# Kernel tuning notes

Hardware: AMD Instinct MI355X
Metric: run time of the kernel (lower is better)

Reference implementation:

```python
import jax, jax.numpy as jnp
import numpy as np

MASK_LOGIT_CONST = 1000000000.0
LN_EPS = 1e-12


def setup_inputs() -> dict:
    key = jax.random.key(0)
    k_in, k_w = jax.random.split(key)
    B, S, H = 8, 2048, 1024
    inputs = jax.random.normal(k_in, (B, S, H), dtype=jnp.float32)
    masks = jnp.ones((B, S, S), dtype=jnp.float32)
    w_match = jax.random.normal(k_w, (2 * H, H), dtype=jnp.float32) * (1.0 / np.sqrt(2 * H))
    b_match = jnp.zeros((H,), dtype=jnp.float32)
    ln_gamma = jnp.ones((H,), dtype=jnp.float32)
    ln_beta = jnp.zeros((H,), dtype=jnp.float32)
    return {"inputs": inputs, "masks": masks, "w_match": w_match,
            "b_match": b_match, "ln_gamma": ln_gamma, "ln_beta": ln_beta}


def reference(inputs, masks, w_match, b_match, ln_gamma, ln_beta):
    H = inputs.shape[-1]
    scale = 1.0 / jnp.sqrt(jnp.asarray(H, dtype=inputs.dtype))
    # self-attention scores [B,S,S] (dropout disabled -> query=key=inputs)
    scores = jnp.einsum('bsh,bth->bst', inputs, inputs) * scale
    # logits_mask: scores*mask + (-C)*(1-mask)
    scores = scores * masks - MASK_LOGIT_CONST * (1.0 - masks)
    probs = jax.nn.softmax(scores, axis=-1)
    context = jnp.einsum('bst,bth->bsh', probs, inputs)
    cat = jnp.concatenate([inputs, context], axis=-1)  # [B,S,2H]
    matching = jnp.einsum('bsk,kh->bsh', cat, w_match) + b_match
    # layernorm over last dim
    mu = jnp.mean(matching, axis=-1, keepdims=True)
    var = jnp.mean((matching - mu) ** 2, axis=-1, keepdims=True)
    normed = (matching - mu) * jax.lax.rsqrt(var + LN_EPS)
    return normed * ln_gamma + ln_beta
```

## Files before the change

kernel.cpp:

```cpp
#include <hip/hip_runtime.h>
#include <hip/hip_bf16.h>


typedef unsigned short ushort_t;
typedef __attribute__((ext_vector_type(8))) short short8;
typedef __attribute__((ext_vector_type(4))) float float4v;

__device__ inline float b2f(unsigned int u) {
    union { unsigned int i; float f; } v; v.i = u << 16; return v.f;
}
__device__ inline ushort_t f2b(float f) {
    __hip_bfloat16 h = __float2bfloat16(f);
    return __builtin_bit_cast(ushort_t, h);
}

__device__ inline void gload_lds16(const ushort_t* g, ushort_t* lds) {
    __builtin_amdgcn_global_load_lds(
        (const __attribute__((address_space(1))) unsigned int*)g,
        (__attribute__((address_space(3))) unsigned int*)lds, 16, 0, 0);
}

#define BM 128
#define BN 128
#define BK 64

template<int EPI>
__global__ __launch_bounds__(256, 2)
void gemm_bt(const ushort_t* __restrict__ A, const ushort_t* __restrict__ A2, int kSplit,
             const ushort_t* __restrict__ B,
             int M, int N, int K, int lda, int ldb, int ldc,
             long aBS, long bBS, long cBS,
             const float* __restrict__ mask, long mBS, float scale,
             float* __restrict__ rowsum,
             const float* __restrict__ bias,
             ushort_t* __restrict__ outb, float* __restrict__ outf)
{
    __shared__ __align__(16) ushort_t As[BM * BK];
    __shared__ __align__(16) ushort_t Bs[BN * BK];

    const int tid = threadIdx.x;
    const int z = blockIdx.z;
    A  += (size_t)z * aBS;
    A2 += (size_t)z * aBS;
    B  += (size_t)z * bBS;
    if (EPI == 1) mask += (size_t)z * mBS;
    if (EPI == 1 || EPI == 2) rowsum += (size_t)z * M;
    if (EPI != 3) outb += (size_t)z * cBS;

    const int bm = blockIdx.y * BM;
    const int bn = blockIdx.x * BN;
    const int wave = tid >> 6, lane = tid & 63;
    const int wm = (wave >> 1) * 64, wn = (wave & 1) * 64;
    const int q = lane >> 4, l15 = lane & 15;
    const int lrow = lane >> 3;
    const int cswz = (lane & 7) ^ lrow;

    float4v acc[4][4];
#pragma unroll
    for (int i = 0; i < 4; i++)
#pragma unroll
        for (int j = 0; j < 4; j++) acc[i][j] = (float4v){0.f, 0.f, 0.f, 0.f};

    for (int k0 = 0; k0 < K; k0 += BK) {
        const ushort_t* aSrc = A;
        int ka = k0;
        if (k0 >= kSplit) { aSrc = A2; ka = k0 - kSplit; }
#pragma unroll
        for (int j = 0; j < 4; j++) {
            const int p = wave * 4 + j;
            const int ro = p * 8 + lrow;
            gload_lds16(aSrc + (size_t)(bm + ro) * lda + ka + cswz * 8, &As[p * 512]);
            gload_lds16(B    + (size_t)(bn + ro) * ldb + k0 + cswz * 8, &Bs[p * 512]);
        }
        __syncthreads();
#pragma unroll
        for (int kk = 0; kk < BK; kk += 32) {
            short8 af[4], bfv[4];
#pragma unroll
            for (int mi = 0; mi < 4; mi++) {
                const int lr = wm + mi * 16 + l15;
                const int kc = (kk >> 3) + q;
                af[mi] = *(const short8*)(&As[lr * 64 + ((kc ^ (lr & 7)) << 3)]);
            }
#pragma unroll
            for (int ni = 0; ni < 4; ni++) {
                const int lr = wn + ni * 16 + l15;
                const int kc = (kk >> 3) + q;
                bfv[ni] = *(const short8*)(&Bs[lr * 64 + ((kc ^ (lr & 7)) << 3)]);
            }
#pragma unroll
            for (int mi = 0; mi < 4; mi++)
#pragma unroll
                for (int ni = 0; ni < 4; ni++)
                    acc[mi][ni] = __builtin_amdgcn_mfma_f32_16x16x32_bf16(
                        af[mi], bfv[ni], acc[mi][ni], 0, 0, 0);
        }
        __syncthreads();
    }

#pragma unroll
    for (int mi = 0; mi < 4; mi++) {
#pragma unroll
        for (int r = 0; r < 4; r++) {
            const int row = bm + wm + mi * 16 + q * 4 + r;
            const size_t ro = (size_t)row * ldc;
            float rsinv = 1.f;
            if (EPI == 2) rsinv = 1.0f / rowsum[row];
            float s = 0.f;
#pragma unroll
            for (int ni = 0; ni < 4; ni++) {
                const int col = bn + wn + ni * 16 + l15;
                float v = acc[mi][ni][r];
                if (EPI == 1) {
                    const float m = mask[(size_t)row * N + col];
                    v = __expf(v * scale * m - 1e9f * (1.0f - m));
                    s += v;
                    outb[ro + col] = f2b(v);
                } else if (EPI == 2) {
                    outb[ro + col] = f2b(v * rsinv);
                } else {
                    outf[ro + col] = v + bias[col];
                }
            }
            if (EPI == 1) {
                s += __shfl_xor(s, 8);
                s += __shfl_xor(s, 4);
                s += __shfl_xor(s, 2);
                s += __shfl_xor(s, 1);
                if (l15 == 0) atomicAdd(&rowsum[row], s);
            }
        }
    }
}

__global__ __launch_bounds__(256)
void conv_trans(const float* __restrict__ in, ushort_t* __restrict__ outT,
                ushort_t* __restrict__ outS, int R, int C)
{
    __shared__ float tile[64][65];
    const int tx = threadIdx.x & 15, ty = threadIdx.x >> 4;
    const size_t zoff = (size_t)blockIdx.z * R * C;
    const int r0 = blockIdx.y * 64, c0 = blockIdx.x * 64;
#pragma unroll
    for (int j = 0; j < 4; j++) {
        const int r = ty + j * 16;
        const float4 v = *(const float4*)(in + zoff + (size_t)(r0 + r) * C + c0 + tx * 4);
        tile[r][tx * 4 + 0] = v.x;
        tile[r][tx * 4 + 1] = v.y;
        tile[r][tx * 4 + 2] = v.z;
        tile[r][tx * 4 + 3] = v.w;
        if (outS) {
            ushort4 o;
            o.x = f2b(v.x); o.y = f2b(v.y); o.z = f2b(v.z); o.w = f2b(v.w);
            *(ushort4*)(outS + zoff + (size_t)(r0 + r) * C + c0 + tx * 4) = o;
        }
    }
    __syncthreads();
    ushort_t* tp = outT + zoff;
#pragma unroll
    for (int j = 0; j < 4; j++) {
        const int cc = ty + j * 16;
        ushort4 o;
        o.x = f2b(tile[tx * 4 + 0][cc]);
        o.y = f2b(tile[tx * 4 + 1][cc]);
        o.z = f2b(tile[tx * 4 + 2][cc]);
        o.w = f2b(tile[tx * 4 + 3][cc]);
        *(ushort4*)(tp + (size_t)(c0 + cc) * R + r0 + tx * 4) = o;
    }
}

__global__ __launch_bounds__(256)
void ln_k(const float* __restrict__ Mt, const float* __restrict__ gamma,
          const float* __restrict__ beta, float* __restrict__ out)
{
    const size_t row = blockIdx.x;
    const int tid = threadIdx.x;
    const float4 v = *(const float4*)(Mt + row * 1024 + tid * 4);
    float s  = v.x + v.y + v.z + v.w;
    float s2 = v.x * v.x + v.y * v.y + v.z * v.z + v.w * v.w;
#pragma unroll
    for (int off = 32; off > 0; off >>= 1) {
        s  += __shfl_down(s, off);
        s2 += __shfl_down(s2, off);
    }
    __shared__ float red[8];
    const int wave = tid >> 6, lane = tid & 63;
    if (lane == 0) { red[wave] = s; red[4 + wave] = s2; }
    __syncthreads();
    s  = red[0] + red[1] + red[2] + red[3];
    s2 = red[4] + red[5] + red[6] + red[7];
    const float mu  = s * (1.0f / 1024.0f);
    const float var = s2 * (1.0f / 1024.0f) - mu * mu;
    const float rinv = rsqrtf(var + 1e-12f);
    const float4 g = *(const float4*)(gamma + tid * 4);
    const float4 b = *(const float4*)(beta + tid * 4);
    float4 o;
    o.x = (v.x - mu) * rinv * g.x + b.x;
    o.y = (v.y - mu) * rinv * g.y + b.y;
    o.z = (v.z - mu) * rinv * g.z + b.z;
    o.w = (v.w - mu) * rinv * g.w + b.w;
    *(float4*)(out + row * 1024 + tid * 4) = o;
}

extern "C" void kernel_launch(void* const* d_in, const int* in_sizes, int n_in,
                              void* d_out, int out_size, void* d_ws, size_t ws_size,
                              hipStream_t stream)
{
    const float* X     = (const float*)d_in[0];
    const float* masks = (const float*)d_in[1];
    const float* Wm    = (const float*)d_in[2];
    const float* bias  = (const float*)d_in[3];
    const float* gamma = (const float*)d_in[4];
    const float* beta  = (const float*)d_in[5];
    float* out = (float*)d_out;
    char* ws = (char*)d_ws;

    const int B = 8, S = 2048, H = 1024;

    ushort_t* Xb  = (ushort_t*)(ws);
    ushort_t* XT  = (ushort_t*)(ws + 33554432);
    ushort_t* WT  = (ushort_t*)(ws + 67108864);
    ushort_t* E   = (ushort_t*)(ws + 71303168);
    float*    rs  = (float*)   (ws + 138412032);
    ushort_t* CTX = (ushort_t*)(ws + 138477568);
    float* matching = (float*)E;

    conv_trans<<<dim3(16, 32, 8), 256, 0, stream>>>(X, XT, Xb, S, H);
    conv_trans<<<dim3(16, 32, 1), 256, 0, stream>>>(Wm, WT, nullptr, 2 * H, H);
    hipMemsetAsync(rs, 0, (size_t)B * S * sizeof(float), stream);

    const float scale = 0.03125f;

    gemm_bt<1><<<dim3(16, 16, 8), 256, 0, stream>>>(
        Xb, Xb, 1 << 30, Xb,
        S, S, H, H, H, S,
        (long)S * H, (long)S * H, (long)S * S,
        masks, (long)S * S, scale, rs, nullptr, E, nullptr);

    gemm_bt<2><<<dim3(8, 16, 8), 256, 0, stream>>>(
        E, E, 1 << 30, XT,
        S, H, S, S, S, H,
        (long)S * S, (long)H * S, (long)S * H,
        nullptr, 0, 1.0f, rs, nullptr, CTX, nullptr);

    gemm_bt<3><<<dim3(8, 128, 1), 256, 0, stream>>>(
        Xb, CTX, H, WT,
        B * S, H, 2 * H, H, 2 * H, H,
        0, 0, 0,
        nullptr, 0, 1.0f, nullptr, bias, nullptr, matching);

    ln_k<<<B * S, 256, 0, stream>>>(matching, gamma, beta, out);
}
```

Baseline: 552.8 us.

## Use FP8 MFMA for score GEMM and store matching output as bf16

Quantizes X to FP8 e4m3 during the conversion pass and computes the QK^T score GEMM with a dedicated FP8 MFMA kernel (K-tile 128), keeping the fused mask/exp/rowsum epilogue. The matching GEMM now writes bf16 instead of fp32 and layernorm reads bf16, which halves that intermediate's traffic. Grid axes are swapped so blockIdx.x walks M tiles, which changes block scheduling order. FP8 scores carry much larger quantization error than bf16, and the softmax exponent amplifies it, so accuracy may suffer. The FP8 buffer reuses the CTX workspace before CTX is written.

```diff
diff --git a/kernel.cpp b/kernel.cpp
--- a/kernel.cpp
+++ b/kernel.cpp
@@ -1,5 +1,6 @@
 #include <hip/hip_runtime.h>
 #include <hip/hip_bf16.h>
+#include <hip/hip_fp8.h>
 
 
 typedef unsigned short ushort_t;
@@ -13,8 +14,11 @@
     __hip_bfloat16 h = __float2bfloat16(f);
     return __builtin_bit_cast(ushort_t, h);
 }
-
-__device__ inline void gload_lds16(const ushort_t* g, ushort_t* lds) {
+__device__ inline unsigned char f2e4(float f) {
+    return __hip_fp8_e4m3(f).__x;
+}
+
+__device__ inline void gload_lds16(const void* g, void* lds) {
     __builtin_amdgcn_global_load_lds(
         (const __attribute__((address_space(1))) unsigned int*)g,
         (__attribute__((address_space(3))) unsigned int*)lds, 16, 0, 0);
@@ -30,10 +34,9 @@
              const ushort_t* __restrict__ B,
              int M, int N, int K, int lda, int ldb, int ldc,
              long aBS, long bBS, long cBS,
-             const float* __restrict__ mask, long mBS, float scale,
-             float* __restrict__ rowsum,
+             const float* __restrict__ rowsum,
              const float* __restrict__ bias,
-             ushort_t* __restrict__ outb, float* __restrict__ outf)
+             ushort_t* __restrict__ outb)
 {
     __shared__ __align__(16) ushort_t As[BM * BK];
     __shared__ __align__(16) ushort_t Bs[BN * BK];
@@ -43,12 +46,11 @@
     A  += (size_t)z * aBS;
     A2 += (size_t)z * aBS;
     B  += (size_t)z * bBS;
-    if (EPI == 1) mask += (size_t)z * mBS;
-    if (EPI == 1 || EPI == 2) rowsum += (size_t)z * M;
-    if (EPI != 3) outb += (size_t)z * cBS;
-
-    const int bm = blockIdx.y * BM;
-    const int bn = blockIdx.x * BN;
+    if (EPI == 2) rowsum += (size_t)z * M;
+    outb += (size_t)z * cBS;
+
+    const int bm = blockIdx.x * BM;
+    const int bn = blockIdx.y * BN;
     const int wave = tid >> 6, lane = tid & 63;
     const int wm = (wave >> 1) * 64, wn = (wave & 1) * 64;
     const int q = lane >> 4, l15 = lane & 15;
@@ -76,16 +78,15 @@
 #pragma unroll
         for (int kk = 0; kk < BK; kk += 32) {
             short8 af[4], bfv[4];
+            const int kc = (kk >> 3) + q;
 #pragma unroll
             for (int mi = 0; mi < 4; mi++) {
                 const int lr = wm + mi * 16 + l15;
-                const int kc = (kk >> 3) + q;
                 af[mi] = *(const short8*)(&As[lr * 64 + ((kc ^ (lr & 7)) << 3)]);
             }
 #pragma unroll
             for (int ni = 0; ni < 4; ni++) {
                 const int lr = wn + ni * 16 + l15;
-                const int kc = (kk >> 3) + q;
                 bfv[ni] = *(const short8*)(&Bs[lr * 64 + ((kc ^ (lr & 7)) << 3)]);
             }
 #pragma unroll
@@ -106,36 +107,107 @@
             const size_t ro = (size_t)row * ldc;
             float rsinv = 1.f;
             if (EPI == 2) rsinv = 1.0f / rowsum[row];
-            float s = 0.f;
 #pragma unroll
             for (int ni = 0; ni < 4; ni++) {
                 const int col = bn + wn + ni * 16 + l15;
                 float v = acc[mi][ni][r];
-                if (EPI == 1) {
-                    const float m = mask[(size_t)row * N + col];
-                    v = __expf(v * scale * m - 1e9f * (1.0f - m));
-                    s += v;
-                    outb[ro + col] = f2b(v);
-                } else if (EPI == 2) {
-                    outb[ro + col] = f2b(v * rsinv);
-                } else {
-                    outf[ro + col] = v + bias[col];
-                }
+                if (EPI == 2) outb[ro + col] = f2b(v * rsinv);
+                else          outb[ro + col] = f2b(v + bias[col]);
             }
-            if (EPI == 1) {
-                s += __shfl_xor(s, 8);
-                s += __shfl_xor(s, 4);
-                s += __shfl_xor(s, 2);
-                s += __shfl_xor(s, 1);
-                if (l15 == 0) atomicAdd(&rowsum[row], s);
+        }
+    }
+}
+
+__global__ __launch_bounds__(256, 2)
+void gemm1_fp8(const unsigned char* __restrict__ X8,
+               const float* __restrict__ mask,
+               float* __restrict__ rowsum,
+               ushort_t* __restrict__ E)
+{
+    __shared__ __align__(16) unsigned char As[128 * 128];
+    __shared__ __align__(16) unsigned char Bs[128 * 128];
+
+    const int tid = threadIdx.x;
+    const int z = blockIdx.z;
+    const unsigned char* Xz = X8 + (size_t)z * 2048 * 1024;
+    const float* mz = mask + (size_t)z * 2048 * 2048;
+    float* rsz = rowsum + (size_t)z * 2048;
+    ushort_t* Ez = E + (size_t)z * 2048 * 2048;
+
+    const int bm = blockIdx.x * 128;
+    const int bn = blockIdx.y * 128;
+    const int wave = tid >> 6, lane = tid & 63;
+    const int wm = (wave >> 1) * 64, wn = (wave & 1) * 64;
+    const int q = lane >> 4, l15 = lane & 15;
+    const int rx = l15 & 7;
+    const int lrow = lane >> 3;
+    const int cswz = (lane & 7) ^ lrow;
+
+    float4v acc[4][4];
+#pragma unroll
+    for (int i = 0; i < 4; i++)
+#pragma unroll
+        for (int j = 0; j < 4; j++) acc[i][j] = (float4v){0.f, 0.f, 0.f, 0.f};
+
+    for (int k0 = 0; k0 < 1024; k0 += 128) {
+#pragma unroll
+        for (int j = 0; j < 4; j++) {
+            const int p = wave * 4 + j;
+            const int ro = p * 8 + lrow;
+            gload_lds16(Xz + (size_t)(bm + ro) * 1024 + k0 + cswz * 16, &As[p * 1024]);
+            gload_lds16(Xz + (size_t)(bn + ro) * 1024 + k0 + cswz * 16, &Bs[p * 1024]);
+        }
+        __syncthreads();
+#pragma unroll
+        for (int kk = 0; kk < 128; kk += 32) {
+            const int g = (kk >> 3) + q;
+            const int co = (((g >> 1) ^ rx) << 4) + ((g & 1) << 3);
+            long af[4], bfv[4];
+#pragma unroll
+            for (int mi = 0; mi < 4; mi++)
+                af[mi] = *(const long*)(&As[(wm + mi * 16 + l15) * 128 + co]);
+#pragma unroll
+            for (int ni = 0; ni < 4; ni++)
+                bfv[ni] = *(const long*)(&Bs[(wn + ni * 16 + l15) * 128 + co]);
+#pragma unroll
+            for (int mi = 0; mi < 4; mi++)
+#pragma unroll
+                for (int ni = 0; ni < 4; ni++)
+                    acc[mi][ni] = __builtin_amdgcn_mfma_f32_16x16x32_fp8_fp8(
+                        af[mi], bfv[ni], acc[mi][ni], 0, 0, 0);
+        }
+        __syncthreads();
+    }
+
+    const float scale = 0.03125f;
+#pragma unroll
+    for (int mi = 0; mi < 4; mi++) {
+#pragma unroll
+        for (int r = 0; r < 4; r++) {
+            const int row = bm + wm + mi * 16 + q * 4 + r;
+            const size_t ro = (size_t)row * 2048;
+            float s = 0.f;
+#pragma unroll
+            for (int ni = 0; ni < 4; ni++) {
+                const int col = bn + wn + ni * 16 + l15;
+                const float m = mz[ro + col];
+                float v = __expf(acc[mi][ni][r] * scale * m - 1e9f * (1.0f - m));
+                s += v;
+                Ez[ro + col] = f2b(v);
             }
+            s += __shfl_xor(s, 8);
+            s += __shfl_xor(s, 4);
+            s += __shfl_xor(s, 2);
+            s += __shfl_xor(s, 1);
+            if (l15 == 0) atomicAdd(&rsz[row], s);
         }
     }
 }
 
 __global__ __launch_bounds__(256)
 void conv_trans(const float* __restrict__ in, ushort_t* __restrict__ outT,
-                ushort_t* __restrict__ outS, int R, int C)
+                ushort_t* __restrict__ outS, unsigned char* __restrict__ outQ,
+                int R, int C)
 {
     __shared__ float tile[64][65];
     const int tx = threadIdx.x & 15, ty = threadIdx.x >> 4;
@@ -153,6 +225,9 @@
             ushort4 o;
             o.x = f2b(v.x); o.y = f2b(v.y); o.z = f2b(v.z); o.w = f2b(v.w);
             *(ushort4*)(outS + zoff + (size_t)(r0 + r) * C + c0 + tx * 4) = o;
+            uchar4 p;
+            p.x = f2e4(v.x); p.y = f2e4(v.y); p.z = f2e4(v.z); p.w = f2e4(v.w);
+            *(uchar4*)(outQ + zoff + (size_t)(r0 + r) * C + c0 + tx * 4) = p;
         }
     }
     __syncthreads();
@@ -170,14 +245,15 @@
 }
 
 __global__ __launch_bounds__(256)
-void ln_k(const float* __restrict__ Mt, const float* __restrict__ gamma,
+void ln_k(const ushort_t* __restrict__ Mt, const float* __restrict__ gamma,
           const float* __restrict__ beta, float* __restrict__ out)
 {
     const size_t row = blockIdx.x;
     const int tid = threadIdx.x;
-    const float4 v = *(const float4*)(Mt + row * 1024 + tid * 4);
-    float s  = v.x + v.y + v.z + v.w;
-    float s2 = v.x * v.x + v.y * v.y + v.z * v.z + v.w * v.w;
+    const ushort4 u = *(const ushort4*)(Mt + row * 1024 + tid * 4);
+    float x0 = b2f(u.x), x1 = b2f(u.y), x2 = b2f(u.z), x3 = b2f(u.w);
+    float s  = x0 + x1 + x2 + x3;
+    float s2 = x0 * x0 + x1 * x1 + x2 * x2 + x3 * x3;
 #pragma unroll
     for (int off = 32; off > 0; off >>= 1) {
         s  += __shfl_down(s, off);
@@ -195,10 +271,10 @@
     const float4 g = *(const float4*)(gamma + tid * 4);
     const float4 b = *(const float4*)(beta + tid * 4);
     float4 o;
-    o.x = (v.x - mu) * rinv * g.x + b.x;
-    o.y = (v.y - mu) * rinv * g.y + b.y;
-    o.z = (v.z - mu) * rinv * g.z + b.z;
-    o.w = (v.w - mu) * rinv * g.w + b.w;
+    o.x = (x0 - mu) * rinv * g.x + b.x;
+    o.y = (x1 - mu) * rinv * g.y + b.y;
+    o.z = (x2 - mu) * rinv * g.z + b.z;
+    o.w = (x3 - mu) * rinv * g.w + b.w;
     *(float4*)(out + row * 1024 + tid * 4) = o;
 }
 
@@ -223,31 +299,26 @@
     ushort_t* E   = (ushort_t*)(ws + 71303168);
     float*    rs  = (float*)   (ws + 138412032);
     ushort_t* CTX = (ushort_t*)(ws + 138477568);
-    float* matching = (float*)E;
-
-    conv_trans<<<dim3(16, 32, 8), 256, 0, stream>>>(X, XT, Xb, S, H);
-    conv_trans<<<dim3(16, 32, 1), 256, 0, stream>>>(Wm, WT, nullptr, 2 * H, H);
+    unsigned char* X8 = (unsigned char*)CTX;
+    ushort_t* matching = E;
+
+    conv_trans<<<dim3(16, 32, 8), 256, 0, stream>>>(X, XT, Xb, X8, S, H);
+    conv_trans<<<dim3(16, 32, 1), 256, 0, stream>>>(Wm, WT, nullptr, nullptr, 2 * H, H);
     hipMemsetAsync(rs, 0, (size_t)B * S * sizeof(float), stream);
 
-    const float scale = 0.03125f;
-
-    gemm_bt<1><<<dim3(16, 16, 8), 256, 0, stream>>>(
-        Xb, Xb, 1 << 30, Xb,
-        S, S, H, H, H, S,
-        (long)S * H, (long)S * H, (long)S * S,
-        masks, (long)S * S, scale, rs, nullptr, E, nullptr);
-
-    gemm_bt<2><<<dim3(8, 16, 8), 256, 0, stream>>>(
+    gemm1_fp8<<<dim3(16, 16, 8), 256, 0, stream>>>(X8, masks, rs, E);
+
+    gemm_bt<2><<<dim3(16, 8, 8), 256, 0, stream>>>(
         E, E, 1 << 30, XT,
         S, H, S, S, S, H,
         (long)S * S, (long)H * S, (long)S * H,
-        nullptr, 0, 1.0f, rs, nullptr, CTX, nullptr);
-
-    gemm_bt<3><<<dim3(8, 128, 1), 256, 0, stream>>>(
+        rs, nullptr, CTX);
+
+    gemm_bt<3><<<dim3(128, 8, 1), 256, 0, stream>>>(
         Xb, CTX, H, WT,
         B * S, H, 2 * H, H, 2 * H, H,
         0, 0, 0,
-        nullptr, 0, 1.0f, nullptr, bias, nullptr, matching);
+        nullptr, bias, matching);
 
     ln_k<<<B * S, 256, 0, stream>>>(matching, gamma, beta, out);
 }
```

Result: faster. 507.0 us (-8.3%).
